# Optimization experiments

Hardware: AMD Instinct MI355X
Metric: run time of the kernel (lower is better)

Reference implementation:

```python
import jax, jax.numpy as jnp
import numpy as np

N_NODES = 50000
N_EDGES = 800000
IN_FEATS = 128
OUT_FEATS = 128


def setup_inputs() -> dict:
    key = jax.random.key(0)
    k1, k2, k3, k4 = jax.random.split(key, 4)
    feature = jax.random.normal(k1, (N_NODES, IN_FEATS), dtype=jnp.float32)
    src = jax.random.randint(k2, (N_EDGES,), 0, N_NODES, dtype=jnp.int64)
    dst = jax.random.randint(k3, (N_EDGES,), 0, N_NODES, dtype=jnp.int64)
    # nn.Linear(in_feats, out_feats): W is [out, in], b is [out]
    bound = 1.0 / np.sqrt(IN_FEATS)
    W = jax.random.uniform(k4, (OUT_FEATS, IN_FEATS), minval=-bound, maxval=bound, dtype=jnp.float32)
    b = jnp.zeros((OUT_FEATS,), dtype=jnp.float32)
    return {"feature": feature, "src": src, "dst": dst, "W": W, "b": b}


def reference(feature, src, dst, W, b):
    # DGL update_all(copy_src('h'), sum('m','h')): h'[v] = sum over edges u->v of h[u]
    n_nodes = feature.shape[0]
    msgs = feature[src]  # [E, in_feats] gather
    agg = jax.ops.segment_sum(msgs, dst, num_segments=n_nodes)  # [N, in_feats]
    # linear: agg @ W.T + b
    return jnp.einsum("ni,oi->no", agg, W) + b
```

## Files before the change

kernel.cpp:

```cpp
#include <hip/hip_runtime.h>
#include <hip/hip_bf16.h>

#define N_FEATS 128
#define SCAN_CHUNK 1024

typedef __attribute__((ext_vector_type(8))) short bf16x8;
typedef __attribute__((ext_vector_type(4))) float f32x4;

__device__ __forceinline__ unsigned short f32_to_bf16_rne(float f) {
    unsigned u = __float_as_uint(f);
    u = u + 0x7FFFu + ((u >> 16) & 1u);
    return (unsigned short)(u >> 16);
}

__global__ void gcn_init(const float* __restrict__ W, float* __restrict__ Wt,
                         const float* __restrict__ feat, unsigned short* __restrict__ featb,
                         int cast_chunks, unsigned short* __restrict__ Wb,
                         int* __restrict__ deg, int n_nodes) {
    int t = blockIdx.x * blockDim.x + threadIdx.x;
    if (t < cast_chunks) {
        const float4* f4 = reinterpret_cast<const float4*>(feat) + (size_t)t * 2;
        float4 x0 = f4[0];
        float4 x1 = f4[1];
        ushort4 o0, o1;
        o0.x = f32_to_bf16_rne(x0.x); o0.y = f32_to_bf16_rne(x0.y);
        o0.z = f32_to_bf16_rne(x0.z); o0.w = f32_to_bf16_rne(x0.w);
        o1.x = f32_to_bf16_rne(x1.x); o1.y = f32_to_bf16_rne(x1.y);
        o1.z = f32_to_bf16_rne(x1.z); o1.w = f32_to_bf16_rne(x1.w);
        reinterpret_cast<ushort4*>(featb)[(size_t)t * 2 + 0] = o0;
        reinterpret_cast<ushort4*>(featb)[(size_t)t * 2 + 1] = o1;
    }
    int t2 = t - cast_chunks;
    const int wcast = (Wb != nullptr) ? (N_FEATS * N_FEATS / 8) : 0;
    if (t2 >= 0 && t2 < wcast) {
        const float4* f4 = reinterpret_cast<const float4*>(W) + (size_t)t2 * 2;
        float4 x0 = f4[0];
        float4 x1 = f4[1];
        ushort4 o0, o1;
        o0.x = f32_to_bf16_rne(x0.x); o0.y = f32_to_bf16_rne(x0.y);
        o0.z = f32_to_bf16_rne(x0.z); o0.w = f32_to_bf16_rne(x0.w);
        o1.x = f32_to_bf16_rne(x1.x); o1.y = f32_to_bf16_rne(x1.y);
        o1.z = f32_to_bf16_rne(x1.z); o1.w = f32_to_bf16_rne(x1.w);
        reinterpret_cast<ushort4*>(Wb)[(size_t)t2 * 2 + 0] = o0;
        reinterpret_cast<ushort4*>(Wb)[(size_t)t2 * 2 + 1] = o1;
    }
    int t3 = t2 - wcast;
    if (t3 >= 0 && t3 < N_FEATS * N_FEATS) {
        int o = t3 >> 7;
        int i = t3 & 127;
        Wt[i * N_FEATS + o] = W[o * N_FEATS + i];
    }
    int u = t3 - N_FEATS * N_FEATS;
    if (u >= 0 && u < n_nodes) deg[u] = 0;
}

__global__ void gcn_hist_pos(const int* __restrict__ src, const int* __restrict__ dst,
                             int* __restrict__ deg, int* __restrict__ pos,
                             int n_edges, int n_nodes) {
    int e = blockIdx.x * blockDim.x + threadIdx.x;
    if (e >= n_edges) return;
    int d = dst[e];
    int s = src[e];
    if ((unsigned)d < (unsigned)n_nodes && (unsigned)s < (unsigned)n_nodes)
        pos[e] = atomicAdd(&deg[d], 1);
}

__global__ void gcn_hist(const int* __restrict__ src, const int* __restrict__ dst,
                         int* __restrict__ deg, int n_edges, int n_nodes) {
    int e = blockIdx.x * blockDim.x + threadIdx.x;
    if (e >= n_edges) return;
    int d = dst[e];
    int s = src[e];
    if ((unsigned)d < (unsigned)n_nodes && (unsigned)s < (unsigned)n_nodes)
        atomicAdd(&deg[d], 1);
}

__launch_bounds__(256)
__global__ void gcn_scan_part(const int* __restrict__ deg, int* __restrict__ chunk_sum, int n) {
    const int t = threadIdx.x;
    const int base = blockIdx.x * SCAN_CHUNK;
    int sum = 0;
#pragma unroll
    for (int k = 0; k < 4; ++k) {
        int idx = base + k * 256 + t;
        if (idx < n) sum += deg[idx];
    }
    for (int d = 1; d < 64; d <<= 1) sum += __shfl_xor(sum, d, 64);
    __shared__ int wsum[4];
    if ((t & 63) == 0) wsum[t >> 6] = sum;
    __syncthreads();
    if (t == 0) chunk_sum[blockIdx.x] = wsum[0] + wsum[1] + wsum[2] + wsum[3];
}

__launch_bounds__(256)
__global__ void gcn_scan_final(const int* __restrict__ deg, const int* __restrict__ chunk_sum,
                               int* __restrict__ row_start, int* __restrict__ cursor,
                               int n, int nchunks) {
    const int t = threadIdx.x;
    const int b = blockIdx.x;

    int v = 0;
    for (int j = t; j < b; j += 256) v += chunk_sum[j];
    for (int d = 1; d < 64; d <<= 1) v += __shfl_xor(v, d, 64);
    __shared__ int owsum[4];
    __shared__ int s_off;
    if ((t & 63) == 0) owsum[t >> 6] = v;
    __syncthreads();
    if (t == 0) s_off = owsum[0] + owsum[1] + owsum[2] + owsum[3];
    __syncthreads();
    const int chunk_off = s_off;

    const int base = b * SCAN_CHUNK;
    const int idx0 = base + t * 4;
    int x[4];
#pragma unroll
    for (int k = 0; k < 4; ++k) {
        int idx = idx0 + k;
        x[k] = (idx < n) ? deg[idx] : 0;
    }
    const int tsum = x[0] + x[1] + x[2] + x[3];

    const int lane = t & 63, w = t >> 6;
    int inc = tsum;
    for (int d = 1; d < 64; d <<= 1) {
        int sv = __shfl_up(inc, d, 64);
        if (lane >= d) inc += sv;
    }
    __shared__ int wsum[4];
    if (lane == 63) wsum[w] = inc;
    __syncthreads();
    int woff = 0;
    for (int i = 0; i < w; ++i) woff += wsum[i];

    int run = chunk_off + woff + inc - tsum;
#pragma unroll
    for (int k = 0; k < 4; ++k) {
        int idx = idx0 + k;
        if (idx < n) {
            row_start[idx] = run;
            if (cursor) cursor[idx] = 0;
        }
        run += x[k];
    }

    if (t == 0 && b == nchunks - 1)
        row_start[n] = chunk_off + wsum[0] + wsum[1] + wsum[2] + wsum[3];
}

__global__ void gcn_build_csr_pos(const int* __restrict__ src, const int* __restrict__ dst,
                                  const int* __restrict__ row_start, const int* __restrict__ pos,
                                  int* __restrict__ csr_src, int n_edges, int n_nodes) {
    int e = blockIdx.x * blockDim.x + threadIdx.x;
    if (e >= n_edges) return;
    int d = dst[e];
    int s = src[e];
    if ((unsigned)d >= (unsigned)n_nodes || (unsigned)s >= (unsigned)n_nodes) return;
    csr_src[row_start[d] + pos[e]] = s;
}

__global__ void gcn_build_csr(const int* __restrict__ src, const int* __restrict__ dst,
                              const int* __restrict__ row_start, int* __restrict__ cursor,
                              int* __restrict__ csr_src, int n_edges, int n_nodes) {
    int e = blockIdx.x * blockDim.x + threadIdx.x;
    if (e >= n_edges) return;
    int d = dst[e];
    int s = src[e];
    if ((unsigned)d >= (unsigned)n_nodes || (unsigned)s >= (unsigned)n_nodes) return;
    int p = atomicAdd(&cursor[d], 1);
    csr_src[row_start[d] + p] = s;
}

#define BACC(acc, v)                                              \
    do {                                                          \
        unsigned uu;                                              \
        uu = (v).x;                                               \
        acc[0] += __uint_as_float(uu << 16);                      \
        acc[1] += __uint_as_float(uu & 0xFFFF0000u);              \
        uu = (v).y;                                               \
        acc[2] += __uint_as_float(uu << 16);                      \
        acc[3] += __uint_as_float(uu & 0xFFFF0000u);              \
        uu = (v).z;                                               \
        acc[4] += __uint_as_float(uu << 16);                      \
        acc[5] += __uint_as_float(uu & 0xFFFF0000u);              \
        uu = (v).w;                                               \
        acc[6] += __uint_as_float(uu << 16);                      \
        acc[7] += __uint_as_float(uu & 0xFFFF0000u);              \
    } while (0)

__launch_bounds__(256)
__global__ void gcn_aggregate_bf16(const uint4* __restrict__ featb,
                                   const int* __restrict__ row_start,
                                   const int* __restrict__ csr_src,
                                   float* __restrict__ out, int n_nodes) {
    int node = blockIdx.x * 4 + (threadIdx.x >> 6);
    if (node >= n_nodes) return;
    const int l = threadIdx.x & 63;
    const int qw = l >> 4;
    const int ql = l & 15;
    int beg = row_start[node];
    int end = row_start[node + 1];

    float a0[8] = {0,0,0,0,0,0,0,0};
    float a1[8] = {0,0,0,0,0,0,0,0};
    float a2[8] = {0,0,0,0,0,0,0,0};
    float a3[8] = {0,0,0,0,0,0,0,0};

    int i = beg;
    for (; i + 16 <= end; i += 16) {
        int s0 = csr_src[i + qw];
        int s1 = csr_src[i + 4 + qw];
        int s2 = csr_src[i + 8 + qw];
        int s3 = csr_src[i + 12 + qw];
        uint4 v0 = featb[(size_t)s0 * 16 + ql];
        uint4 v1 = featb[(size_t)s1 * 16 + ql];
        uint4 v2 = featb[(size_t)s2 * 16 + ql];
        uint4 v3 = featb[(size_t)s3 * 16 + ql];
        BACC(a0, v0);
        BACC(a1, v1);
        BACC(a2, v2);
        BACC(a3, v3);
    }
    for (; i + 4 <= end; i += 4) {
        int s = csr_src[i + qw];
        uint4 v = featb[(size_t)s * 16 + ql];
        BACC(a0, v);
    }
    int rem = end - i;
    if (qw < rem) {
        int s = csr_src[i + qw];
        uint4 v = featb[(size_t)s * 16 + ql];
        BACC(a0, v);
    }

    float r[8];
#pragma unroll
    for (int k = 0; k < 8; ++k) {
        r[k] = a0[k] + a1[k] + a2[k] + a3[k];
        r[k] += __shfl_xor(r[k], 16, 64);
        r[k] += __shfl_xor(r[k], 32, 64);
    }

    if (qw == 0) {
        float4* o4 = reinterpret_cast<float4*>(out + (size_t)node * N_FEATS + ql * 8);
        o4[0] = make_float4(r[0], r[1], r[2], r[3]);
        o4[1] = make_float4(r[4], r[5], r[6], r[7]);
    }
}

__launch_bounds__(256)
__global__ void gcn_aggregate(const float* __restrict__ feat,
                              const int* __restrict__ row_start,
                              const int* __restrict__ csr_src,
                              float* __restrict__ out, int n_nodes) {
    int node = blockIdx.x * 4 + (threadIdx.x >> 6);
    if (node >= n_nodes) return;
    const int l = threadIdx.x & 63;
    const int q = l & 31;
    const int h = l >> 5;
    int beg = row_start[node];
    int end = row_start[node + 1];
    const float4* f4 = reinterpret_cast<const float4*>(feat);

    float4 a0 = make_float4(0.f, 0.f, 0.f, 0.f);
    float4 a1 = a0, a2 = a0, a3 = a0;
    int i = beg;
    for (; i + 8 <= end; i += 8) {
        int s0 = csr_src[i + h];
        int s1 = csr_src[i + 2 + h];
        int s2 = csr_src[i + 4 + h];
        int s3 = csr_src[i + 6 + h];
        float4 v0 = f4[(size_t)s0 * 32 + q];
        float4 v1 = f4[(size_t)s1 * 32 + q];
        float4 v2 = f4[(size_t)s2 * 32 + q];
        float4 v3 = f4[(size_t)s3 * 32 + q];
        a0.x += v0.x; a0.y += v0.y; a0.z += v0.z; a0.w += v0.w;
        a1.x += v1.x; a1.y += v1.y; a1.z += v1.z; a1.w += v1.w;
        a2.x += v2.x; a2.y += v2.y; a2.z += v2.z; a2.w += v2.w;
        a3.x += v3.x; a3.y += v3.y; a3.z += v3.z; a3.w += v3.w;
    }
    for (; i + 2 <= end; i += 2) {
        int s0 = csr_src[i + h];
        float4 v0 = f4[(size_t)s0 * 32 + q];
        a0.x += v0.x; a0.y += v0.y; a0.z += v0.z; a0.w += v0.w;
    }
    if (i < end && h == 0) {
        int s = csr_src[i];
        float4 v = f4[(size_t)s * 32 + q];
        a0.x += v.x; a0.y += v.y; a0.z += v.z; a0.w += v.w;
    }

    float4 acc = make_float4(a0.x + a1.x + a2.x + a3.x,
                             a0.y + a1.y + a2.y + a3.y,
                             a0.z + a1.z + a2.z + a3.z,
                             a0.w + a1.w + a2.w + a3.w);
    acc.x += __shfl_xor(acc.x, 32, 64);
    acc.y += __shfl_xor(acc.y, 32, 64);
    acc.z += __shfl_xor(acc.z, 32, 64);
    acc.w += __shfl_xor(acc.w, 32, 64);

    if (h == 0)
        reinterpret_cast<float4*>(out)[(size_t)node * 32 + q] = acc;
}

__global__ void gcn_scatter_add(const float* __restrict__ feat,
                                const int* __restrict__ src,
                                const int* __restrict__ dst,
                                float* __restrict__ agg,
                                int n_edges, int n_nodes) {
    long long tid = (long long)blockIdx.x * blockDim.x + threadIdx.x;
    int e = (int)(tid >> 5);
    if (e >= n_edges) return;
    int j = (int)(tid & 31);
    int s = src[e];
    int d = dst[e];
    if ((unsigned)s >= (unsigned)n_nodes || (unsigned)d >= (unsigned)n_nodes) return;
    const float4 v = *reinterpret_cast<const float4*>(feat + (size_t)s * N_FEATS + j * 4);
    float* p = agg + (size_t)d * N_FEATS + j * 4;
    atomicAdd(p + 0, v.x);
    atomicAdd(p + 1, v.y);
    atomicAdd(p + 2, v.z);
    atomicAdd(p + 3, v.w);
}

__launch_bounds__(256)
__global__ void gcn_gemm_mfma(float* __restrict__ out,
                              const unsigned short* __restrict__ Wb,
                              const float* __restrict__ bias,
                              int n_nodes) {
    const long long gtid = (long long)blockIdx.x * blockDim.x + threadIdx.x;
    const int wave = (int)(gtid >> 6);
    const int row0 = wave * 16;
    if (row0 >= n_nodes) return;
    const int l = (int)(threadIdx.x & 63);
    const int lr = l & 15;
    const int kb = l >> 4;

    bf16x8 afrag[4] = {};
    if (row0 + lr < n_nodes) {
        const float* aptr = out + (size_t)(row0 + lr) * N_FEATS + kb * 8;
#pragma unroll
        for (int kk = 0; kk < 4; ++kk) {
            float4 x0 = *reinterpret_cast<const float4*>(aptr + kk * 32);
            float4 x1 = *reinterpret_cast<const float4*>(aptr + kk * 32 + 4);
            bf16x8 af;
            af[0] = (short)f32_to_bf16_rne(x0.x);
            af[1] = (short)f32_to_bf16_rne(x0.y);
            af[2] = (short)f32_to_bf16_rne(x0.z);
            af[3] = (short)f32_to_bf16_rne(x0.w);
            af[4] = (short)f32_to_bf16_rne(x1.x);
            af[5] = (short)f32_to_bf16_rne(x1.y);
            af[6] = (short)f32_to_bf16_rne(x1.z);
            af[7] = (short)f32_to_bf16_rne(x1.w);
            afrag[kk] = af;
        }
    }

    f32x4 acc[8];
#pragma unroll
    for (int nt = 0; nt < 8; ++nt) acc[nt] = (f32x4){0.f, 0.f, 0.f, 0.f};

#pragma unroll
    for (int nt = 0; nt < 8; ++nt) {
        const unsigned short* wp = Wb + (size_t)(nt * 16 + lr) * N_FEATS + kb * 8;
#pragma unroll
        for (int kk = 0; kk < 4; ++kk) {
            bf16x8 bfrag = *reinterpret_cast<const bf16x8*>(wp + kk * 32);
            acc[nt] = __builtin_amdgcn_mfma_f32_16x16x32_bf16(afrag[kk], bfrag, acc[nt], 0, 0, 0);
        }
    }

#pragma unroll
    for (int nt = 0; nt < 8; ++nt) {
        const int col = nt * 16 + lr;
        const float bb = bias[col];
#pragma unroll
        for (int j = 0; j < 4; ++j) {
            const int r = row0 + kb * 4 + j;
            if (r < n_nodes)
                out[(size_t)r * N_FEATS + col] = acc[nt][j] + bb;
        }
    }
}

__launch_bounds__(256)
__global__ void gcn_gemm_inplace(float* __restrict__ out,
                                 const float* __restrict__ Wt,
                                 const float* __restrict__ b,
                                 int n_nodes) {
    __shared__ float a_lds[32 * N_FEATS];

    const int t = threadIdx.x;
    const int node0 = blockIdx.x * 32;
    const int rows = min(32, n_nodes - node0);

    float4* a4 = reinterpret_cast<float4*>(a_lds);
    const float4* out4 = reinterpret_cast<const float4*>(out + (size_t)node0 * N_FEATS);
    const int nflt4 = rows * (N_FEATS / 4);
    for (int idx = t; idx < nflt4; idx += 256) a4[idx] = out4[idx];
    __syncthreads();

    const int oq = t & 31;
    const int ng = t >> 5;

    const float4 bb = reinterpret_cast<const float4*>(b)[oq];
    float4 acc[4];
#pragma unroll
    for (int k = 0; k < 4; ++k) acc[k] = bb;

    const float4* Wt4 = reinterpret_cast<const float4*>(Wt);
#pragma unroll 4
    for (int i = 0; i < N_FEATS; ++i) {
        const float4 w = Wt4[i * 32 + oq];
#pragma unroll
        for (int k = 0; k < 4; ++k) {
            const float a = a_lds[(ng * 4 + k) * N_FEATS + i];
            acc[k].x += a * w.x;
            acc[k].y += a * w.y;
            acc[k].z += a * w.z;
            acc[k].w += a * w.w;
        }
    }

    __syncthreads();

#pragma unroll
    for (int k = 0; k < 4; ++k) {
        const int r = ng * 4 + k;
        if (r < rows) {
            reinterpret_cast<float4*>(out + (size_t)(node0 + r) * N_FEATS)[oq] = acc[k];
        }
    }
}

extern "C" void kernel_launch(void* const* d_in, const int* in_sizes, int n_in,
                              void* d_out, int out_size, void* d_ws, size_t ws_size,
                              hipStream_t stream) {
    const float* feature = (const float*)d_in[0];
    const int*   src     = (const int*)d_in[1];
    const int*   dst     = (const int*)d_in[2];
    const float* W       = (const float*)d_in[3];
    const float* b       = (const float*)d_in[4];
    float* out = (float*)d_out;

    const int n_nodes = in_sizes[0] / N_FEATS;
    const int n_edges = in_sizes[1];
    const int nchunks = (n_nodes + SCAN_CHUNK - 1) / SCAN_CHUNK;

    char* ws = (char*)d_ws;
    size_t off = 0;
    auto take = [&](size_t bytes) -> char* {
        char* p = ws + off;
        off = (off + bytes + 255) & ~(size_t)255;
        return p;
    };
    float* Wt        = (float*)take((size_t)N_FEATS * N_FEATS * sizeof(float));
    int*   deg       = (int*)  take((size_t)n_nodes * sizeof(int));
    int*   row_start = (int*)  take(((size_t)n_nodes + 1) * sizeof(int));
    int*   chunk_sum = (int*)  take((size_t)nchunks * sizeof(int));
    int*   csr_src   = (int*)  take((size_t)n_edges * sizeof(int));
    const size_t off_common = off;

    unsigned short* featb = (unsigned short*)take((size_t)n_nodes * N_FEATS * sizeof(unsigned short));
    unsigned short* Wb    = (unsigned short*)take((size_t)N_FEATS * N_FEATS * sizeof(unsigned short));
    int* posA2 = (int*)take((size_t)n_edges * sizeof(int));
    const bool tierA2 = (off <= ws_size);
    off = off_common;
    int* posA = (int*)take((size_t)n_edges * sizeof(int));
    const bool tierA = !tierA2 && (off <= ws_size);
    off = off_common;
    int* cursor = (int*)take((size_t)n_nodes * sizeof(int));
    const bool tierB = !tierA2 && !tierA && (off <= ws_size);

    if (tierA2 || tierA || tierB) {
        const int cast_chunks = tierA2 ? (n_nodes * (N_FEATS / 8)) : 0;
        const int wcast = tierA2 ? (N_FEATS * N_FEATS / 8) : 0;
        const int init_elems = cast_chunks + wcast + N_FEATS * N_FEATS + n_nodes;
        gcn_init<<<(init_elems + 255) / 256, 256, 0, stream>>>(
            W, Wt, feature, featb, cast_chunks,
            tierA2 ? Wb : (unsigned short*)nullptr, deg, n_nodes);

        const int eblocks = (n_edges + 255) / 256;
        int* pos = tierA2 ? posA2 : posA;
        if (tierA2 || tierA) {
            gcn_hist_pos<<<eblocks, 256, 0, stream>>>(src, dst, deg, pos, n_edges, n_nodes);
        } else {
            gcn_hist<<<eblocks, 256, 0, stream>>>(src, dst, deg, n_edges, n_nodes);
        }
        gcn_scan_part<<<nchunks, 256, 0, stream>>>(deg, chunk_sum, n_nodes);
        gcn_scan_final<<<nchunks, 256, 0, stream>>>(deg, chunk_sum, row_start,
                                                    (tierA2 || tierA) ? (int*)nullptr : cursor,
                                                    n_nodes, nchunks);
        if (tierA2 || tierA) {
            gcn_build_csr_pos<<<eblocks, 256, 0, stream>>>(
                src, dst, row_start, pos, csr_src, n_edges, n_nodes);
        } else {
            gcn_build_csr<<<eblocks, 256, 0, stream>>>(
                src, dst, row_start, cursor, csr_src, n_edges, n_nodes);
        }
        if (tierA2) {
            gcn_aggregate_bf16<<<(n_nodes + 3) / 4, 256, 0, stream>>>(
                reinterpret_cast<const uint4*>(featb), row_start, csr_src, out, n_nodes);
        } else {
            gcn_aggregate<<<(n_nodes + 3) / 4, 256, 0, stream>>>(
                feature, row_start, csr_src, out, n_nodes);
        }
    } else {
        gcn_init<<<(N_FEATS * N_FEATS + 255) / 256, 256, 0, stream>>>(
            W, Wt, feature, (unsigned short*)nullptr, 0, (unsigned short*)nullptr, deg, 0);
        hipMemsetAsync(d_out, 0, (size_t)n_nodes * N_FEATS * sizeof(float), stream);
        long long total = (long long)n_edges * 32;
        gcn_scatter_add<<<(int)((total + 255) / 256), 256, 0, stream>>>(
            feature, src, dst, out, n_edges, n_nodes);
    }

    if (tierA2) {
        const long long nthr = (long long)((n_nodes + 15) / 16) * 64;
        gcn_gemm_mfma<<<(int)((nthr + 255) / 256), 256, 0, stream>>>(out, Wb, b, n_nodes);
    } else {
        gcn_gemm_inplace<<<(n_nodes + 31) / 32, 256, 0, stream>>>(out, Wt, b, n_nodes);
    }
}
```

Before: 124.9 us.

## Transform features before aggregation and fuse bias into aggregate epilogue

```diff
diff --git a/kernel.cpp b/kernel.cpp
--- a/kernel.cpp
+++ b/kernel.cpp
@@ -14,44 +14,94 @@
 }
 
 __global__ void gcn_init(const float* __restrict__ W, float* __restrict__ Wt,
-                         const float* __restrict__ feat, unsigned short* __restrict__ featb,
-                         int cast_chunks, unsigned short* __restrict__ Wb,
+                         unsigned short* __restrict__ Wb,
                          int* __restrict__ deg, int n_nodes) {
     int t = blockIdx.x * blockDim.x + threadIdx.x;
-    if (t < cast_chunks) {
-        const float4* f4 = reinterpret_cast<const float4*>(feat) + (size_t)t * 2;
-        float4 x0 = f4[0];
-        float4 x1 = f4[1];
-        ushort4 o0, o1;
-        o0.x = f32_to_bf16_rne(x0.x); o0.y = f32_to_bf16_rne(x0.y);
-        o0.z = f32_to_bf16_rne(x0.z); o0.w = f32_to_bf16_rne(x0.w);
-        o1.x = f32_to_bf16_rne(x1.x); o1.y = f32_to_bf16_rne(x1.y);
-        o1.z = f32_to_bf16_rne(x1.z); o1.w = f32_to_bf16_rne(x1.w);
-        reinterpret_cast<ushort4*>(featb)[(size_t)t * 2 + 0] = o0;
-        reinterpret_cast<ushort4*>(featb)[(size_t)t * 2 + 1] = o1;
-    }
-    int t2 = t - cast_chunks;
-    const int wcast = (Wb != nullptr) ? (N_FEATS * N_FEATS / 8) : 0;
-    if (t2 >= 0 && t2 < wcast) {
-        const float4* f4 = reinterpret_cast<const float4*>(W) + (size_t)t2 * 2;
-        float4 x0 = f4[0];
-        float4 x1 = f4[1];
-        ushort4 o0, o1;
-        o0.x = f32_to_bf16_rne(x0.x); o0.y = f32_to_bf16_rne(x0.y);
-        o0.z = f32_to_bf16_rne(x0.z); o0.w = f32_to_bf16_rne(x0.w);
-        o1.x = f32_to_bf16_rne(x1.x); o1.y = f32_to_bf16_rne(x1.y);
-        o1.z = f32_to_bf16_rne(x1.z); o1.w = f32_to_bf16_rne(x1.w);
-        reinterpret_cast<ushort4*>(Wb)[(size_t)t2 * 2 + 0] = o0;
-        reinterpret_cast<ushort4*>(Wb)[(size_t)t2 * 2 + 1] = o1;
-    }
-    int t3 = t2 - wcast;
-    if (t3 >= 0 && t3 < N_FEATS * N_FEATS) {
-        int o = t3 >> 7;
-        int i = t3 & 127;
-        Wt[i * N_FEATS + o] = W[o * N_FEATS + i];
-    }
-    int u = t3 - N_FEATS * N_FEATS;
-    if (u >= 0 && u < n_nodes) deg[u] = 0;
+    if (t < N_FEATS * N_FEATS / 8) {
+        if (Wb) {
+            const float4* f4 = reinterpret_cast<const float4*>(W) + (size_t)t * 2;
+            float4 x0 = f4[0];
+            float4 x1 = f4[1];
+            ushort4 o0, o1;
+            o0.x = f32_to_bf16_rne(x0.x); o0.y = f32_to_bf16_rne(x0.y);
+            o0.z = f32_to_bf16_rne(x0.z); o0.w = f32_to_bf16_rne(x0.w);
+            o1.x = f32_to_bf16_rne(x1.x); o1.y = f32_to_bf16_rne(x1.y);
+            o1.z = f32_to_bf16_rne(x1.z); o1.w = f32_to_bf16_rne(x1.w);
+            reinterpret_cast<ushort4*>(Wb)[(size_t)t * 2 + 0] = o0;
+            reinterpret_cast<ushort4*>(Wb)[(size_t)t * 2 + 1] = o1;
+        }
+        return;
+    }
+    int t2 = t - N_FEATS * N_FEATS / 8;
+    if (t2 < N_FEATS * N_FEATS) {
+        if (Wt) {
+            int o = t2 >> 7;
+            int i = t2 & 127;
+            Wt[i * N_FEATS + o] = W[o * N_FEATS + i];
+        }
+        return;
+    }
+    int u = t2 - N_FEATS * N_FEATS;
+    if (u < n_nodes) deg[u] = 0;
+}
+
+__launch_bounds__(256)
+__global__ void gcn_transform_mfma(const float* __restrict__ feat,
+                                   const unsigned short* __restrict__ Wb,
+                                   unsigned short* __restrict__ Y,
+                                   int n_nodes) {
+    const long long gtid = (long long)blockIdx.x * blockDim.x + threadIdx.x;
+    const int wave = (int)(gtid >> 6);
+    const int row0 = wave * 16;
+    if (row0 >= n_nodes) return;
+    const int l = (int)(threadIdx.x & 63);
+    const int lr = l & 15;
+    const int kb = l >> 4;
+
+    bf16x8 afrag[4] = {};
+    if (row0 + lr < n_nodes) {
+        const float* aptr = feat + (size_t)(row0 + lr) * N_FEATS + kb * 8;
+#pragma unroll
+        for (int kk = 0; kk < 4; ++kk) {
+            float4 x0 = *reinterpret_cast<const float4*>(aptr + kk * 32);
+            float4 x1 = *reinterpret_cast<const float4*>(aptr + kk * 32 + 4);
+            bf16x8 af;
+            af[0] = (short)f32_to_bf16_rne(x0.x);
+            af[1] = (short)f32_to_bf16_rne(x0.y);
+            af[2] = (short)f32_to_bf16_rne(x0.z);
+            af[3] = (short)f32_to_bf16_rne(x0.w);
+            af[4] = (short)f32_to_bf16_rne(x1.x);
+            af[5] = (short)f32_to_bf16_rne(x1.y);
+            af[6] = (short)f32_to_bf16_rne(x1.z);
+            af[7] = (short)f32_to_bf16_rne(x1.w);
+            afrag[kk] = af;
+        }
+    }
+
+    f32x4 acc[8];
+#pragma unroll
+    for (int nt = 0; nt < 8; ++nt) acc[nt] = (f32x4){0.f, 0.f, 0.f, 0.f};
+
+#pragma unroll
+    for (int nt = 0; nt < 8; ++nt) {
+        const unsigned short* wp = Wb + (size_t)(nt * 16 + lr) * N_FEATS + kb * 8;
+#pragma unroll
+        for (int kk = 0; kk < 4; ++kk) {
+            bf16x8 bfrag = *reinterpret_cast<const bf16x8*>(wp + kk * 32);
+            acc[nt] = __builtin_amdgcn_mfma_f32_16x16x32_bf16(afrag[kk], bfrag, acc[nt], 0, 0, 0);
+        }
+    }
+
+#pragma unroll
+    for (int nt = 0; nt < 8; ++nt) {
+        const int col = nt * 16 + lr;
+#pragma unroll
+        for (int j = 0; j < 4; ++j) {
+            const int r = row0 + kb * 4 + j;
+            if (r < n_nodes)
+                Y[(size_t)r * N_FEATS + col] = f32_to_bf16_rne(acc[nt][j]);
+        }
+    }
 }
 
 __global__ void gcn_hist_pos(const int* __restrict__ src, const int* __restrict__ dst,
@@ -188,9 +238,10 @@
     } while (0)
 
 __launch_bounds__(256)
-__global__ void gcn_aggregate_bf16(const uint4* __restrict__ featb,
+__global__ void gcn_aggregate_bf16(const uint4* __restrict__ Y,
                                    const int* __restrict__ row_start,
                                    const int* __restrict__ csr_src,
+                                   const float* __restrict__ bias,
                                    float* __restrict__ out, int n_nodes) {
     int node = blockIdx.x * 4 + (threadIdx.x >> 6);
     if (node >= n_nodes) return;
@@ -211,10 +262,10 @@
         int s1 = csr_src[i + 4 + qw];
         int s2 = csr_src[i + 8 + qw];
         int s3 = csr_src[i + 12 + qw];
-        uint4 v0 = featb[(size_t)s0 * 16 + ql];
-        uint4 v1 = featb[(size_t)s1 * 16 + ql];
-        uint4 v2 = featb[(size_t)s2 * 16 + ql];
-        uint4 v3 = featb[(size_t)s3 * 16 + ql];
+        uint4 v0 = Y[(size_t)s0 * 16 + ql];
+        uint4 v1 = Y[(size_t)s1 * 16 + ql];
+        uint4 v2 = Y[(size_t)s2 * 16 + ql];
+        uint4 v3 = Y[(size_t)s3 * 16 + ql];
         BACC(a0, v0);
         BACC(a1, v1);
         BACC(a2, v2);
@@ -222,13 +273,13 @@
     }
     for (; i + 4 <= end; i += 4) {
         int s = csr_src[i + qw];
-        uint4 v = featb[(size_t)s * 16 + ql];
+        uint4 v = Y[(size_t)s * 16 + ql];
         BACC(a0, v);
     }
     int rem = end - i;
     if (qw < rem) {
         int s = csr_src[i + qw];
-        uint4 v = featb[(size_t)s * 16 + ql];
+        uint4 v = Y[(size_t)s * 16 + ql];
         BACC(a0, v);
     }
 
@@ -241,9 +292,11 @@
     }
 
     if (qw == 0) {
+        const float4 b0 = *reinterpret_cast<const float4*>(bias + ql * 8);
+        const float4 b1 = *reinterpret_cast<const float4*>(bias + ql * 8 + 4);
         float4* o4 = reinterpret_cast<float4*>(out + (size_t)node * N_FEATS + ql * 8);
-        o4[0] = make_float4(r[0], r[1], r[2], r[3]);
-        o4[1] = make_float4(r[4], r[5], r[6], r[7]);
+        o4[0] = make_float4(r[0] + b0.x, r[1] + b0.y, r[2] + b0.z, r[3] + b0.w);
+        o4[1] = make_float4(r[4] + b1.x, r[5] + b1.y, r[6] + b1.z, r[7] + b1.w);
     }
 }
 
@@ -323,66 +376,6 @@
 }
 
 __launch_bounds__(256)
-__global__ void gcn_gemm_mfma(float* __restrict__ out,
-                              const unsigned short* __restrict__ Wb,
-                              const float* __restrict__ bias,
-                              int n_nodes) {
-    const long long gtid = (long long)blockIdx.x * blockDim.x + threadIdx.x;
-    const int wave = (int)(gtid >> 6);
-    const int row0 = wave * 16;
-    if (row0 >= n_nodes) return;
-    const int l = (int)(threadIdx.x & 63);
-    const int lr = l & 15;
-    const int kb = l >> 4;
-
-    bf16x8 afrag[4] = {};
-    if (row0 + lr < n_nodes) {
-        const float* aptr = out + (size_t)(row0 + lr) * N_FEATS + kb * 8;
-#pragma unroll
-        for (int kk = 0; kk < 4; ++kk) {
-            float4 x0 = *reinterpret_cast<const float4*>(aptr + kk * 32);
-            float4 x1 = *reinterpret_cast<const float4*>(aptr + kk * 32 + 4);
-            bf16x8 af;
-            af[0] = (short)f32_to_bf16_rne(x0.x);
-            af[1] = (short)f32_to_bf16_rne(x0.y);
-            af[2] = (short)f32_to_bf16_rne(x0.z);
-            af[3] = (short)f32_to_bf16_rne(x0.w);
-            af[4] = (short)f32_to_bf16_rne(x1.x);
-            af[5] = (short)f32_to_bf16_rne(x1.y);
-            af[6] = (short)f32_to_bf16_rne(x1.z);
-            af[7] = (short)f32_to_bf16_rne(x1.w);
-            afrag[kk] = af;
-        }
-    }
-
-    f32x4 acc[8];
-#pragma unroll
-    for (int nt = 0; nt < 8; ++nt) acc[nt] = (f32x4){0.f, 0.f, 0.f, 0.f};
-
-#pragma unroll
-    for (int nt = 0; nt < 8; ++nt) {
-        const unsigned short* wp = Wb + (size_t)(nt * 16 + lr) * N_FEATS + kb * 8;
-#pragma unroll
-        for (int kk = 0; kk < 4; ++kk) {
-            bf16x8 bfrag = *reinterpret_cast<const bf16x8*>(wp + kk * 32);
-            acc[nt] = __builtin_amdgcn_mfma_f32_16x16x32_bf16(afrag[kk], bfrag, acc[nt], 0, 0, 0);
-        }
-    }
-
-#pragma unroll
-    for (int nt = 0; nt < 8; ++nt) {
-        const int col = nt * 16 + lr;
-        const float bb = bias[col];
-#pragma unroll
-        for (int j = 0; j < 4; ++j) {
-            const int r = row0 + kb * 4 + j;
-            if (r < n_nodes)
-                out[(size_t)r * N_FEATS + col] = acc[nt][j] + bb;
-        }
-    }
-}
-
-__launch_bounds__(256)
 __global__ void gcn_gemm_inplace(float* __restrict__ out,
                                  const float* __restrict__ Wt,
                                  const float* __restrict__ b,
@@ -460,8 +453,8 @@
     int*   csr_src   = (int*)  take((size_t)n_edges * sizeof(int));
     const size_t off_common = off;
 
-    unsigned short* featb = (unsigned short*)take((size_t)n_nodes * N_FEATS * sizeof(unsigned short));
-    unsigned short* Wb    = (unsigned short*)take((size_t)N_FEATS * N_FEATS * sizeof(unsigned short));
+    unsigned short* Yb = (unsigned short*)take((size_t)n_nodes * N_FEATS * sizeof(unsigned short));
+    unsigned short* Wb = (unsigned short*)take((size_t)N_FEATS * N_FEATS * sizeof(unsigned short));
     int* posA2 = (int*)take((size_t)n_edges * sizeof(int));
     const bool tierA2 = (off <= ws_size);
     off = off_common;
@@ -471,13 +464,18 @@
     int* cursor = (int*)take((size_t)n_nodes * sizeof(int));
     const bool tierB = !tierA2 && !tierA && (off <= ws_size);
 
+    const int init_elems = N_FEATS * N_FEATS / 8 + N_FEATS * N_FEATS + n_nodes;
+
     if (tierA2 || tierA || tierB) {
-        const int cast_chunks = tierA2 ? (n_nodes * (N_FEATS / 8)) : 0;
-        const int wcast = tierA2 ? (N_FEATS * N_FEATS / 8) : 0;
-        const int init_elems = cast_chunks + wcast + N_FEATS * N_FEATS + n_nodes;
         gcn_init<<<(init_elems + 255) / 256, 256, 0, stream>>>(
-            W, Wt, feature, featb, cast_chunks,
+            W, tierA2 ? (float*)nullptr : Wt,
             tierA2 ? Wb : (unsigned short*)nullptr, deg, n_nodes);
+
+        if (tierA2) {
+            const long long nthr = (long long)((n_nodes + 15) / 16) * 64;
+            gcn_transform_mfma<<<(int)((nthr + 255) / 256), 256, 0, stream>>>(
+                feature, Wb, Yb, n_nodes);
+        }
 
         const int eblocks = (n_edges + 255) / 256;
         int* pos = tierA2 ? posA2 : posA;
@@ -499,24 +497,19 @@
         }
         if (tierA2) {
             gcn_aggregate_bf16<<<(n_nodes + 3) / 4, 256, 0, stream>>>(
-                reinterpret_cast<const uint4*>(featb), row_start, csr_src, out, n_nodes);
+                reinterpret_cast<const uint4*>(Yb), row_start, csr_src, b, out, n_nodes);
         } else {
             gcn_aggregate<<<(n_nodes + 3) / 4, 256, 0, stream>>>(
                 feature, row_start, csr_src, out, n_nodes);
+            gcn_gemm_inplace<<<(n_nodes + 31) / 32, 256, 0, stream>>>(out, Wt, b, n_nodes);
         }
     } else {
-        gcn_init<<<(N_FEATS * N_FEATS + 255) / 256, 256, 0, stream>>>(
-            W, Wt, feature, (unsigned short*)nullptr, 0, (unsigned short*)nullptr, deg, 0);
+        gcn_init<<<(init_elems + 255) / 256, 256, 0, stream>>>(
+            W, Wt, (unsigned short*)nullptr, deg, n_nodes);
         hipMemsetAsync(d_out, 0, (size_t)n_nodes * N_FEATS * sizeof(float), stream);
         long long total = (long long)n_edges * 32;
         gcn_scatter_add<<<(int)((total + 255) / 256), 256, 0, stream>>>(
             feature, src, dst, out, n_edges, n_nodes);
-    }
-
-    if (tierA2) {
-        const long long nthr = (long long)((n_nodes + 15) / 16) * 64;
-        gcn_gemm_mfma<<<(int)((nthr + 255) / 256), 256, 0, stream>>>(out, Wb, b, n_nodes);
-    } else {
         gcn_gemm_inplace<<<(n_nodes + 31) / 32, 256, 0, stream>>>(out, Wt, b, n_nodes);
     }
 }
```

After: 124.0 us. No clear change (-0.7%).
